# Kernel optimization log

Measured on AMD Instinct MI355X. Metric: run time of the kernel, lower is better.

The kernel has to match this reference:

```python
import jax, jax.numpy as jnp
import numpy as np

B, S, T, D = 4, 512, 512, 256


def setup_inputs() -> dict:
    key = jax.random.key(0)
    ks = jax.random.split(key, 10)
    scale = 1.0 / np.sqrt(D)
    return {
        "source": jax.random.normal(ks[0], (B, S, D), jnp.float32),
        "target": jax.random.normal(ks[1], (B, T, D), jnp.float32),
        "W_src": jax.random.uniform(ks[2], (D, D), jnp.float32, -scale, scale),
        "b_src": jax.random.uniform(ks[3], (D,), jnp.float32, -scale, scale),
        "W_tgt": jax.random.uniform(ks[4], (D, D), jnp.float32, -scale, scale),
        "b_tgt": jax.random.uniform(ks[5], (D,), jnp.float32, -scale, scale),
        "W_res": jax.random.uniform(ks[6], (D, 1), jnp.float32, -scale, scale),
        "b_res": jax.random.uniform(ks[7], (1,), jnp.float32, -scale, scale),
        "W_prob": jax.random.uniform(ks[8], (D, 2), jnp.float32, -scale, scale),
        "b_prob": jax.random.uniform(ks[9], (2,), jnp.float32, -scale, scale),
    }


def reference(source, target, W_src, b_src, W_tgt, b_tgt, W_res, b_res, W_prob, b_prob):
    # source: (B,S,D), target: (B,T,D)
    src_lin = jnp.einsum("bsd,de->bse", source, W_src) + b_src  # (B,S,D)
    tgt_lin = jnp.einsum("btd,de->bte", target, W_tgt) + b_tgt  # (B,T,D)
    # Bahdanau-style additive attention: (B,T,S,D) broadcast, tanh, D->1
    h = jnp.tanh(src_lin[:, None, :, :] + tgt_lin[:, :, None, :])  # (B,T,S,D)
    genP = jnp.einsum("btsd,d->bts", h, W_res[:, 0]) + b_res[0]     # (B,T,S)
    prob = jax.nn.softmax(jnp.einsum("btd,de->bte", target, W_prob) + b_prob, axis=-1)  # (B,T,2)
    return genP, prob
```

## Files before the change

### kernel.cpp

```cpp
#include <hip/hip_runtime.h>

#define B_ 4
#define S_ 512
#define T_ 512
#define D_ 256
#define NSRC (B_ * S_)
#define K2F 2.8853900817779268f

typedef __attribute__((ext_vector_type(8))) short short8;
typedef __attribute__((ext_vector_type(4))) float f32x4;

__device__ __forceinline__ unsigned short f2bf(float f) {
    union { float f; unsigned u; } v; v.f = f;
    unsigned r = v.u + 0x7FFF + ((v.u >> 16) & 1);
    return (unsigned short)(r >> 16);
}

__global__ __launch_bounds__(256) void prep_kernel(
    const float* __restrict__ src, const float* __restrict__ tgt,
    const float* __restrict__ Wsrc, const float* __restrict__ Wtgt,
    const float* __restrict__ Wp, const float* __restrict__ bp,
    unsigned short* __restrict__ abf, unsigned short* __restrict__ wtb,
    float* __restrict__ out)
{
    __shared__ float tl[64 * 65];
    const int blk = blockIdx.x, tid = threadIdx.x;

    if (blk < 1024) {
        int i4 = blk * 256 + tid;
        const int half = NSRC * D_ / 4;
        const float4* in = (i4 < half) ? (const float4*)src : (const float4*)tgt;
        int j = (i4 < half) ? i4 : i4 - half;
        float4 v = in[j];
        ushort4 o;
        o.x = f2bf(v.x); o.y = f2bf(v.y); o.z = f2bf(v.z); o.w = f2bf(v.w);
        *(ushort4*)&abf[i4 * 4] = o;
    } else if (blk < 1056) {
        int wb = blk - 1024;
        int e = wb >> 4, ti = wb & 15, tr = ti >> 2, tc = ti & 3;
        int r0 = tr * 64, c0 = tc * 64;
        const float* W = e ? Wtgt : Wsrc;
        #pragma unroll
        for (int it = 0; it < 4; it++) {
            int rr = (tid >> 4) + it * 16;
            int cc = (tid & 15) * 4;
            float4 v = *(const float4*)&W[(r0 + rr) * D_ + c0 + cc];
            tl[(cc + 0) * 65 + rr] = v.x;
            tl[(cc + 1) * 65 + rr] = v.y;
            tl[(cc + 2) * 65 + rr] = v.z;
            tl[(cc + 3) * 65 + rr] = v.w;
        }
        __syncthreads();
        #pragma unroll
        for (int it = 0; it < 2; it++) {
            int jj = (tid >> 3) + it * 32;
            int kk = (tid & 7) * 8;
            ushort4 lo, hi;
            lo.x = f2bf(tl[jj * 65 + kk + 0]); lo.y = f2bf(tl[jj * 65 + kk + 1]);
            lo.z = f2bf(tl[jj * 65 + kk + 2]); lo.w = f2bf(tl[jj * 65 + kk + 3]);
            hi.x = f2bf(tl[jj * 65 + kk + 4]); hi.y = f2bf(tl[jj * 65 + kk + 5]);
            hi.z = f2bf(tl[jj * 65 + kk + 6]); hi.w = f2bf(tl[jj * 65 + kk + 7]);
            int idx = (e * 256 + c0 + jj) * D_ + r0 + kk;
            *(ushort4*)&wtb[idx] = lo;
            *(ushort4*)&wtb[idx + 4] = hi;
        }
    } else {
        int row  = (blk - 1056) * 4 + (tid >> 6);
        int lane = tid & 63;
        float p0 = 0.f, p1 = 0.f;
        #pragma unroll
        for (int i = 0; i < 4; i++) {
            int d = lane + i * 64;
            float v = tgt[row * D_ + d];
            float2 w = *(const float2*)&Wp[d * 2];
            p0 = fmaf(v, w.x, p0);
            p1 = fmaf(v, w.y, p1);
        }
        #pragma unroll
        for (int off = 32; off > 0; off >>= 1) {
            p0 += __shfl_down(p0, off, 64);
            p1 += __shfl_down(p1, off, 64);
        }
        if (lane == 0) {
            const float L2E = 1.4426950408889634f;
            float l0 = p0 + bp[0], l1 = p1 + bp[1];
            float e10 = __builtin_amdgcn_exp2f((l1 - l0) * L2E);
            float e01 = __builtin_amdgcn_exp2f((l0 - l1) * L2E);
            out[B_ * T_ * S_ + row * 2 + 0] = __builtin_amdgcn_rcpf(1.f + e10);
            out[B_ * T_ * S_ + row * 2 + 1] = __builtin_amdgcn_rcpf(1.f + e01);
        }
    }
}

__global__ __launch_bounds__(256) void mega_kernel(
    const unsigned short* __restrict__ abf, const unsigned short* __restrict__ wtb,
    const float* __restrict__ bsrc, const float* __restrict__ btgt,
    const float* __restrict__ Wres, const float* __restrict__ bres,
    float* __restrict__ out)
{
    __shared__ float ls[D_ * 33];
    __shared__ float lt[D_ * 33];
    __shared__ float wl[D_];
    __shared__ float c0s;

    const int tid = threadIdx.x;
    const int lane = tid & 63, w = tid >> 6;
    const int s0 = blockIdx.x * 32;
    const int t0 = blockIdx.y * 32;
    const int b  = blockIdx.z;

    wl[tid] = Wres[tid];
    if (w == 0) {
        float s = Wres[lane] + Wres[lane + 64] + Wres[lane + 128] + Wres[lane + 192];
        #pragma unroll
        for (int off = 32; off > 0; off >>= 1) s += __shfl_xor(s, off, 64);
        if (lane == 0) c0s = s + bres[0];
    }

    const int mat = w >> 1;
    const int n = lane & 15, quad = lane >> 4;
    const float* bias = mat ? btgt : bsrc;
    float* lx = mat ? lt : ls;
    const int R = mat ? (NSRC + b * T_ + t0) : (b * S_ + s0);

    short8 af[2][8];
    #pragma unroll
    for (int rg = 0; rg < 2; rg++)
        #pragma unroll
        for (int ks = 0; ks < 8; ks++)
            af[rg][ks] = *(const short8*)&abf[(R + rg * 16 + n) * D_ + ks * 32 + quad * 8];

    const int n0beg = (w & 1) * 8;
    #pragma unroll
    for (int n0 = n0beg; n0 < n0beg + 8; n0++) {
        const unsigned short* bp = &wtb[(mat * 256 + n0 * 16 + n) * D_ + quad * 8];
        short8 bf[8];
        #pragma unroll
        for (int ks = 0; ks < 8; ks++) bf[ks] = *(const short8*)&bp[ks * 32];
        f32x4 acc0 = {0.f, 0.f, 0.f, 0.f};
        f32x4 acc1 = {0.f, 0.f, 0.f, 0.f};
        #pragma unroll
        for (int ks = 0; ks < 8; ks++) {
            acc0 = __builtin_amdgcn_mfma_f32_16x16x32_bf16(af[0][ks], bf[ks], acc0, 0, 0, 0);
            acc1 = __builtin_amdgcn_mfma_f32_16x16x32_bf16(af[1][ks], bf[ks], acc1, 0, 0, 0);
        }
        const int dcol = n0 * 16 + n;
        const float bv = bias[dcol];
        #pragma unroll
        for (int i = 0; i < 4; i++) {
            lx[dcol * 33 + quad * 4 + i]      = __builtin_amdgcn_exp2f((acc0[i] + bv) * K2F);
            lx[dcol * 33 + 16 + quad * 4 + i] = __builtin_amdgcn_exp2f((acc1[i] + bv) * K2F);
        }
    }
    __syncthreads();

    const int m = tid & 15;
    const int g = tid >> 4;
    float a00 = 0.f, a01 = 0.f, a10 = 0.f, a11 = 0.f;

    #pragma unroll 8
    for (int k = 0; k < D_; k++) {
        float2 av = *(const float2*)&ls[k * 33 + 2 * m];
        float2 cv = *(const float2*)&lt[k * 33 + 2 * g];
        float wv = wl[k];
        float r;
        r = __builtin_amdgcn_rcpf(fmaf(cv.x, av.x, 1.f)); a00 = fmaf(wv, r, a00);
        r = __builtin_amdgcn_rcpf(fmaf(cv.x, av.y, 1.f)); a01 = fmaf(wv, r, a01);
        r = __builtin_amdgcn_rcpf(fmaf(cv.y, av.x, 1.f)); a10 = fmaf(wv, r, a10);
        r = __builtin_amdgcn_rcpf(fmaf(cv.y, av.y, 1.f)); a11 = fmaf(wv, r, a11);
    }

    const float C0 = c0s;
    float2 o0, o1;
    o0.x = C0 - 2.f * a00; o0.y = C0 - 2.f * a01;
    o1.x = C0 - 2.f * a10; o1.y = C0 - 2.f * a11;
    *(float2*)&out[(b * T_ + t0 + 2 * g + 0) * S_ + s0 + 2 * m] = o0;
    *(float2*)&out[(b * T_ + t0 + 2 * g + 1) * S_ + s0 + 2 * m] = o1;
}

extern "C" void kernel_launch(void* const* d_in, const int* in_sizes, int n_in,
                              void* d_out, int out_size, void* d_ws, size_t ws_size,
                              hipStream_t stream) {
    const float* source = (const float*)d_in[0];
    const float* target = (const float*)d_in[1];
    const float* W_src  = (const float*)d_in[2];
    const float* b_src  = (const float*)d_in[3];
    const float* W_tgt  = (const float*)d_in[4];
    const float* b_tgt  = (const float*)d_in[5];
    const float* W_res  = (const float*)d_in[6];
    const float* b_res  = (const float*)d_in[7];
    const float* W_prob = (const float*)d_in[8];
    const float* b_prob = (const float*)d_in[9];
    float* out = (float*)d_out;

    unsigned short* abf = (unsigned short*)d_ws;
    unsigned short* wtb = abf + 2 * NSRC * D_;

    prep_kernel<<<1568, 256, 0, stream>>>(source, target, W_src, W_tgt,
                                          W_prob, b_prob, abf, wtb, out);
    mega_kernel<<<dim3(16, 16, 4), 256, 0, stream>>>(abf, wtb, b_src, b_tgt,
                                                     W_res, b_res, out);
}
```

Before: 128.3 us.

## Enlarge output tile to 64x64 and chunk the D dimension through shared memory

Each block now computes a 64x64 (t,s) output tile with 4x4 outputs per thread instead of 32x32 with 2x2. The projection GEMM and exp2 results are produced in four 64-wide D chunks that are staged in shared memory and consumed by the rcp/fma inner loop, with syncs between chunks. The goal is to halve the redundant projection GEMM work per output and raise LDS reuse per loaded value. The cost is a grid of only 256 blocks, which may not fill the GPU's compute units, plus more register pressure and extra barriers.

```diff
diff --git a/kernel.cpp b/kernel.cpp
--- a/kernel.cpp
+++ b/kernel.cpp
@@ -92,21 +92,21 @@
     }
 }
 
-__global__ __launch_bounds__(256) void mega_kernel(
+__global__ __launch_bounds__(256, 1) void mega_kernel(
     const unsigned short* __restrict__ abf, const unsigned short* __restrict__ wtb,
     const float* __restrict__ bsrc, const float* __restrict__ btgt,
     const float* __restrict__ Wres, const float* __restrict__ bres,
     float* __restrict__ out)
 {
-    __shared__ float ls[D_ * 33];
-    __shared__ float lt[D_ * 33];
+    __shared__ float ls[64 * 68];
+    __shared__ float lt[64 * 68];
     __shared__ float wl[D_];
     __shared__ float c0s;
 
     const int tid = threadIdx.x;
     const int lane = tid & 63, w = tid >> 6;
-    const int s0 = blockIdx.x * 32;
-    const int t0 = blockIdx.y * 32;
+    const int s0 = blockIdx.x * 64;
+    const int t0 = blockIdx.y * 64;
     const int b  = blockIdx.z;
 
     wl[tid] = Wres[tid];
@@ -117,65 +117,94 @@
         if (lane == 0) c0s = s + bres[0];
     }
 
-    const int mat = w >> 1;
+    const int mat  = w >> 1;
+    const int half = w & 1;
     const int n = lane & 15, quad = lane >> 4;
     const float* bias = mat ? btgt : bsrc;
     float* lx = mat ? lt : ls;
     const int R = mat ? (NSRC + b * T_ + t0) : (b * S_ + s0);
 
-    short8 af[2][8];
+    short8 af[4][8];
     #pragma unroll
-    for (int rg = 0; rg < 2; rg++)
+    for (int rg = 0; rg < 4; rg++)
         #pragma unroll
         for (int ks = 0; ks < 8; ks++)
             af[rg][ks] = *(const short8*)&abf[(R + rg * 16 + n) * D_ + ks * 32 + quad * 8];
 
-    const int n0beg = (w & 1) * 8;
-    #pragma unroll
-    for (int n0 = n0beg; n0 < n0beg + 8; n0++) {
-        const unsigned short* bp = &wtb[(mat * 256 + n0 * 16 + n) * D_ + quad * 8];
-        short8 bf[8];
-        #pragma unroll
-        for (int ks = 0; ks < 8; ks++) bf[ks] = *(const short8*)&bp[ks * 32];
-        f32x4 acc0 = {0.f, 0.f, 0.f, 0.f};
-        f32x4 acc1 = {0.f, 0.f, 0.f, 0.f};
-        #pragma unroll
-        for (int ks = 0; ks < 8; ks++) {
-            acc0 = __builtin_amdgcn_mfma_f32_16x16x32_bf16(af[0][ks], bf[ks], acc0, 0, 0, 0);
-            acc1 = __builtin_amdgcn_mfma_f32_16x16x32_bf16(af[1][ks], bf[ks], acc1, 0, 0, 0);
-        }
-        const int dcol = n0 * 16 + n;
-        const float bv = bias[dcol];
-        #pragma unroll
-        for (int i = 0; i < 4; i++) {
-            lx[dcol * 33 + quad * 4 + i]      = __builtin_amdgcn_exp2f((acc0[i] + bv) * K2F);
-            lx[dcol * 33 + 16 + quad * 4 + i] = __builtin_amdgcn_exp2f((acc1[i] + bv) * K2F);
-        }
-    }
-    __syncthreads();
-
     const int m = tid & 15;
     const int g = tid >> 4;
-    float a00 = 0.f, a01 = 0.f, a10 = 0.f, a11 = 0.f;
-
-    #pragma unroll 8
-    for (int k = 0; k < D_; k++) {
-        float2 av = *(const float2*)&ls[k * 33 + 2 * m];
-        float2 cv = *(const float2*)&lt[k * 33 + 2 * g];
-        float wv = wl[k];
-        float r;
-        r = __builtin_amdgcn_rcpf(fmaf(cv.x, av.x, 1.f)); a00 = fmaf(wv, r, a00);
-        r = __builtin_amdgcn_rcpf(fmaf(cv.x, av.y, 1.f)); a01 = fmaf(wv, r, a01);
-        r = __builtin_amdgcn_rcpf(fmaf(cv.y, av.x, 1.f)); a10 = fmaf(wv, r, a10);
-        r = __builtin_amdgcn_rcpf(fmaf(cv.y, av.y, 1.f)); a11 = fmaf(wv, r, a11);
+    float acc[4][4];
+    #pragma unroll
+    for (int i = 0; i < 4; i++)
+        #pragma unroll
+        for (int j = 0; j < 4; j++) acc[i][j] = 0.f;
+
+    for (int c = 0; c < 4; c++) {
+        #pragma unroll
+        for (int cgi = 0; cgi < 2; cgi++) {
+            const int cg = half * 2 + cgi;
+            const int gcol = c * 4 + cg;
+            const unsigned short* bptr = &wtb[(mat * 256 + gcol * 16 + n) * D_ + quad * 8];
+            short8 bf[8];
+            #pragma unroll
+            for (int ks = 0; ks < 8; ks++) bf[ks] = *(const short8*)&bptr[ks * 32];
+            const int dloc = cg * 16 + n;
+            const float bv = bias[gcol * 16 + n];
+            #pragma unroll
+            for (int rg = 0; rg < 4; rg++) {
+                f32x4 a4 = {0.f, 0.f, 0.f, 0.f};
+                #pragma unroll
+                for (int ks = 0; ks < 8; ks++)
+                    a4 = __builtin_amdgcn_mfma_f32_16x16x32_bf16(af[rg][ks], bf[ks], a4, 0, 0, 0);
+                float4 o;
+                o.x = __builtin_amdgcn_exp2f((a4[0] + bv) * K2F);
+                o.y = __builtin_amdgcn_exp2f((a4[1] + bv) * K2F);
+                o.z = __builtin_amdgcn_exp2f((a4[2] + bv) * K2F);
+                o.w = __builtin_amdgcn_exp2f((a4[3] + bv) * K2F);
+                *(float4*)&lx[dloc * 68 + rg * 16 + quad * 4] = o;
+            }
+        }
+        __syncthreads();
+
+        const float* wp = &wl[c * 64];
+        #pragma unroll 8
+        for (int k = 0; k < 64; k++) {
+            float4 av = *(const float4*)&ls[k * 68 + 4 * m];
+            float4 cv = *(const float4*)&lt[k * 68 + 4 * g];
+            float wv = wp[k];
+            float a0 = av.x, a1 = av.y, a2 = av.z, a3 = av.w;
+            float c0 = cv.x, c1 = cv.y, c2 = cv.z, c3 = cv.w;
+            float r;
+            r = __builtin_amdgcn_rcpf(fmaf(c0, a0, 1.f)); acc[0][0] = fmaf(wv, r, acc[0][0]);
+            r = __builtin_amdgcn_rcpf(fmaf(c0, a1, 1.f)); acc[0][1] = fmaf(wv, r, acc[0][1]);
+            r = __builtin_amdgcn_rcpf(fmaf(c0, a2, 1.f)); acc[0][2] = fmaf(wv, r, acc[0][2]);
+            r = __builtin_amdgcn_rcpf(fmaf(c0, a3, 1.f)); acc[0][3] = fmaf(wv, r, acc[0][3]);
+            r = __builtin_amdgcn_rcpf(fmaf(c1, a0, 1.f)); acc[1][0] = fmaf(wv, r, acc[1][0]);
+            r = __builtin_amdgcn_rcpf(fmaf(c1, a1, 1.f)); acc[1][1] = fmaf(wv, r, acc[1][1]);
+            r = __builtin_amdgcn_rcpf(fmaf(c1, a2, 1.f)); acc[1][2] = fmaf(wv, r, acc[1][2]);
+            r = __builtin_amdgcn_rcpf(fmaf(c1, a3, 1.f)); acc[1][3] = fmaf(wv, r, acc[1][3]);
+            r = __builtin_amdgcn_rcpf(fmaf(c2, a0, 1.f)); acc[2][0] = fmaf(wv, r, acc[2][0]);
+            r = __builtin_amdgcn_rcpf(fmaf(c2, a1, 1.f)); acc[2][1] = fmaf(wv, r, acc[2][1]);
+            r = __builtin_amdgcn_rcpf(fmaf(c2, a2, 1.f)); acc[2][2] = fmaf(wv, r, acc[2][2]);
+            r = __builtin_amdgcn_rcpf(fmaf(c2, a3, 1.f)); acc[2][3] = fmaf(wv, r, acc[2][3]);
+            r = __builtin_amdgcn_rcpf(fmaf(c3, a0, 1.f)); acc[3][0] = fmaf(wv, r, acc[3][0]);
+            r = __builtin_amdgcn_rcpf(fmaf(c3, a1, 1.f)); acc[3][1] = fmaf(wv, r, acc[3][1]);
+            r = __builtin_amdgcn_rcpf(fmaf(c3, a2, 1.f)); acc[3][2] = fmaf(wv, r, acc[3][2]);
+            r = __builtin_amdgcn_rcpf(fmaf(c3, a3, 1.f)); acc[3][3] = fmaf(wv, r, acc[3][3]);
+        }
+        __syncthreads();
     }
 
     const float C0 = c0s;
-    float2 o0, o1;
-    o0.x = C0 - 2.f * a00; o0.y = C0 - 2.f * a01;
-    o1.x = C0 - 2.f * a10; o1.y = C0 - 2.f * a11;
-    *(float2*)&out[(b * T_ + t0 + 2 * g + 0) * S_ + s0 + 2 * m] = o0;
-    *(float2*)&out[(b * T_ + t0 + 2 * g + 1) * S_ + s0 + 2 * m] = o1;
+    #pragma unroll
+    for (int i = 0; i < 4; i++) {
+        float4 o;
+        o.x = C0 - 2.f * acc[i][0];
+        o.y = C0 - 2.f * acc[i][1];
+        o.z = C0 - 2.f * acc[i][2];
+        o.w = C0 - 2.f * acc[i][3];
+        *(float4*)&out[(b * T_ + t0 + 4 * g + i) * S_ + s0 + 4 * m] = o;
+    }
 }
 
 extern "C" void kernel_launch(void* const* d_in, const int* in_sizes, int n_in,
@@ -198,6 +227,6 @@
 
     prep_kernel<<<1568, 256, 0, stream>>>(source, target, W_src, W_tgt,
                                           W_prob, b_prob, abf, wtb, out);
-    mega_kernel<<<dim3(16, 16, 4), 256, 0, stream>>>(abf, wtb, b_src, b_tgt,
-                                                     W_res, b_res, out);
-}
+    mega_kernel<<<dim3(8, 8, 4), 256, 0, stream>>>(abf, wtb, b_src, b_tgt,
+                                                   W_res, b_res, out);
+}
```

New measurement: 126.5 us. About the same (-1.4%).
